# Performance work log

Hardware: AMD Instinct MI355X
Metric: run time of the kernel (lower is better)

The kernel has to match this reference:

```python
import jax, jax.numpy as jnp
import numpy as np
from jax import lax

VOCAB = 32000
D = 256      # d_model
N = 16       # n_neurons
NL = 6       # n_layers
DS = 16      # d_state
DC = 4       # d_conv
DI = 512     # d_inner = expand * d_model
DTR = 16     # dt_rank = ceil(D/16)
NH = 4       # attention heads
HD = D // NH
B, L = 1, 128


def setup_inputs() -> dict:
    key = jax.random.key(0)
    ks = list(jax.random.split(key, 32))
    it = iter(ks)

    def rn(shape, scale):
        return jax.random.normal(next(it), shape, jnp.float32) * scale

    p = {}
    p["x"] = jax.random.randint(next(it), (B, L), 0, VOCAB, dtype=jnp.int32)
    p["embedding"] = rn((VOCAB, D), 0.02)
    p["norm1_w"] = jnp.ones((NL, D)); p["norm1_b"] = jnp.zeros((NL, D))
    p["norm2_w"] = jnp.ones((NL, D)); p["norm2_b"] = jnp.zeros((NL, D))
    # Mamba params (stacked over layers)
    p["in_proj_w"] = rn((NL, 2 * DI, D), D ** -0.5)
    p["conv_w"] = rn((NL, DI, DC), DC ** -0.5)
    p["conv_b"] = jnp.zeros((NL, DI))
    p["x_proj_w"] = rn((NL, DTR + 2 * DS, DI), DI ** -0.5)
    p["dt_proj_w"] = rn((NL, DI, DTR), DTR ** -0.5)
    dt0 = jax.random.uniform(next(it), (NL, DI), jnp.float32, 1e-3, 1e-1)
    p["dt_proj_b"] = jnp.log(jnp.expm1(dt0))  # inverse softplus init
    p["A_log"] = jnp.log(jnp.tile(jnp.arange(1.0, DS + 1.0, dtype=jnp.float32), (NL, DI, 1)))
    p["skip_D"] = jnp.ones((NL, DI))
    p["out_proj_w"] = rn((NL, D, DI), DI ** -0.5)
    # cross-neuron MHA params
    p["attn_in_w"] = rn((NL, 3 * D, D), D ** -0.5)
    p["attn_in_b"] = jnp.zeros((NL, 3 * D))
    p["attn_out_w"] = rn((NL, D, D), D ** -0.5)
    p["attn_out_b"] = jnp.zeros((NL, D))
    p["norm_f_w"] = jnp.ones((D,)); p["norm_f_b"] = jnp.zeros((D,))
    p["head_b"] = jnp.zeros((VOCAB,))
    return p


def _ln(x, w, b):
    m = x.mean(-1, keepdims=True)
    v = ((x - m) ** 2).mean(-1, keepdims=True)
    return (x - m) * lax.rsqrt(v + 1e-5) * w + b


def _mamba(x, ipw, cw, cb, xpw, dpw, dpb, alog, dskip, opw):
    # x: (BN, L, D)
    BN, Ls, _ = x.shape
    xz = x @ ipw.T                       # (BN, L, 2*DI)
    u, z = xz[..., :DI], xz[..., DI:]
    # depthwise causal conv1d, kernel DC, left-pad DC-1
    uc = lax.conv_general_dilated(
        u.swapaxes(1, 2), cw[:, None, :], (1,), [(DC - 1, 0)],
        dimension_numbers=("NCH", "OIH", "NCH"), feature_group_count=DI)
    u = jax.nn.silu(uc + cb[None, :, None]).swapaxes(1, 2)  # (BN, L, DI)
    xdbl = u @ xpw.T                     # (BN, L, DTR+2*DS)
    dt = jax.nn.softplus(xdbl[..., :DTR] @ dpw.T + dpb)     # (BN, L, DI)
    Bm = xdbl[..., DTR:DTR + DS]
    Cm = xdbl[..., DTR + DS:]
    A = -jnp.exp(alog)                   # (DI, DS)

    def step(h, ins):
        dt_t, b_t, c_t, u_t = ins        # (BN,DI) (BN,DS) (BN,DS) (BN,DI)
        h = jnp.exp(dt_t[..., None] * A) * h + (dt_t * u_t)[..., None] * b_t[:, None, :]
        return h, jnp.einsum("bds,bs->bd", h, c_t)

    h0 = jnp.zeros((BN, DI, DS), x.dtype)
    _, ys = lax.scan(step, h0, (dt.swapaxes(0, 1), Bm.swapaxes(0, 1),
                                Cm.swapaxes(0, 1), u.swapaxes(0, 1)))
    y = ys.swapaxes(0, 1) + u * dskip
    return (y * jax.nn.silu(z)) @ opw.T


def _mha(x, iw, ib, ow, ob):
    # x: (B*L, N, D); self-attention across neurons
    Bq, S, _ = x.shape
    qkv = x @ iw.T + ib
    q, k, v = jnp.split(qkv, 3, axis=-1)
    q = q.reshape(Bq, S, NH, HD); k = k.reshape(Bq, S, NH, HD); v = v.reshape(Bq, S, NH, HD)
    att = jax.nn.softmax(jnp.einsum("bqhd,bkhd->bhqk", q, k) / np.float32(np.sqrt(HD)), axis=-1)
    o = jnp.einsum("bhqk,bkhd->bqhd", att, v).reshape(Bq, S, D)
    return o @ ow.T + ob


def reference(x, embedding, norm1_w, norm1_b, norm2_w, norm2_b, in_proj_w, conv_w,
              conv_b, x_proj_w, dt_proj_w, dt_proj_b, A_log, skip_D, out_proj_w,
              attn_in_w, attn_in_b, attn_out_w, attn_out_b, norm_f_w, norm_f_b, head_b):
    Bb, Ll = x.shape
    h = embedding[x]                                             # (B, L, D)
    h = jnp.broadcast_to(h[:, None], (Bb, N, Ll, D)).reshape(Bb * N, Ll, D)
    for i in range(NL):
        h = h + _mamba(_ln(h, norm1_w[i], norm1_b[i]), in_proj_w[i], conv_w[i],
                       conv_b[i], x_proj_w[i], dt_proj_w[i], dt_proj_b[i],
                       A_log[i], skip_D[i], out_proj_w[i])
        xc = _ln(h, norm2_w[i], norm2_b[i]).reshape(Bb, N, Ll, D)
        xc = xc.transpose(0, 2, 1, 3).reshape(Bb * Ll, N, D)
        co = _mha(xc, attn_in_w[i], attn_in_b[i], attn_out_w[i], attn_out_b[i])
        h = h + co.reshape(Bb, Ll, N, D).transpose(0, 2, 1, 3).reshape(Bb * N, Ll, D)
    h = h.reshape(Bb, N, Ll, D).mean(axis=1)                     # avg over neurons
    return _ln(h, norm_f_w, norm_f_b) @ embedding.T + head_b     # tied head
```

## Files before the change

### kernel.cpp

```cpp
#include <hip/hip_runtime.h>

constexpr int SEQ    = 128;
constexpr int NVOCAB = 32000;

constexpr size_t O_HA = 0;
constexpr size_t O_HB = O_HA + (size_t)SEQ*256;
constexpr size_t O_U  = O_HB + (size_t)SEQ*256;
constexpr size_t O_DT = O_U  + (size_t)SEQ*512;
constexpr size_t O_ZS = O_DT + (size_t)SEQ*512;
constexpr size_t O_BC = O_ZS + (size_t)SEQ*512;
constexpr size_t O_YG = O_BC + (size_t)SEQ*32;
constexpr size_t O_AH = O_YG + (size_t)SEQ*512;

__device__ __forceinline__ float wsum(float p) {
    #pragma unroll
    for (int m = 1; m < 64; m <<= 1) p += __shfl_xor(p, m);
    return p;
}
__device__ __forceinline__ float dot4(float4 a, float4 b) {
    return a.x*b.x + a.y*b.y + a.z*b.z + a.w*b.w;
}

template<int MR, int KK>
__device__ __forceinline__ void gemmX(
    const float* __restrict__ Wg, const float* __restrict__ A, int AS,
    float* __restrict__ dest, int DS,
    const float* __restrict__ addsrc, int ASS, const float* __restrict__ bias)
{
    const int lane = threadIdx.x & 63;
    const int wv   = threadIdx.x >> 6;
    const int tq = lane & 3, cs = lane >> 2;
    const int c  = wv*16 + cs;
    const float* Wp = Wg + (size_t)c*KK + tq*8;
    float acc[MR];
    #pragma unroll
    for (int r = 0; r < MR; ++r) acc[r] = 0.0f;

    float4 w0a = *(const float4*)(Wp);
    float4 w0b = *(const float4*)(Wp + 4);
    float4 w1a, w1b;
    #pragma unroll
    for (int kc = 0; kc < KK; kc += 64) {
        if (kc + 32 < KK) {
            w1a = *(const float4*)(Wp + kc + 32);
            w1b = *(const float4*)(Wp + kc + 36);
        }
        #pragma unroll
        for (int r = 0; r < MR; ++r) {
            float4 a0 = *(const float4*)&A[r*AS + kc + tq*8];
            float4 a1 = *(const float4*)&A[r*AS + kc + tq*8 + 4];
            acc[r] += dot4(a0, w0a) + dot4(a1, w0b);
        }
        if (kc + 64 < KK) {
            w0a = *(const float4*)(Wp + kc + 64);
            w0b = *(const float4*)(Wp + kc + 68);
        }
        if (kc + 32 < KK) {
            #pragma unroll
            for (int r = 0; r < MR; ++r) {
                float4 a0 = *(const float4*)&A[r*AS + kc + 32 + tq*8];
                float4 a1 = *(const float4*)&A[r*AS + kc + 36 + tq*8];
                acc[r] += dot4(a0, w1a) + dot4(a1, w1b);
            }
        }
    }
    #pragma unroll
    for (int r = 0; r < MR; ++r) {
        float v = acc[r];
        v += __shfl_xor(v, 1);
        v += __shfl_xor(v, 2);
        acc[r] = v;
    }
    if (tq == 0) {
        #pragma unroll
        for (int r = 0; r < MR; ++r) {
            float v = acc[r];
            if (bias)   v += bias[c];
            if (addsrc) v += addsrc[r*ASS + c];
            dest[r*DS + c] = v;
        }
    }
}

__device__ __forceinline__ void ln_row(const float* __restrict__ src, float* __restrict__ dst,
                                       const float* __restrict__ w, const float* __restrict__ b)
{
    int lane = threadIdx.x & 63;
    float4 x = *(const float4*)&src[lane*4];
    float sm = wsum(x.x + x.y + x.z + x.w);
    float mean = sm * (1.0f/256.0f);
    float d0 = x.x-mean, d1 = x.y-mean, d2 = x.z-mean, d3 = x.w-mean;
    float var = wsum(d0*d0 + d1*d1 + d2*d2 + d3*d3) * (1.0f/256.0f);
    float rstd = rsqrtf(var + 1e-5f);
    float4 ww = *(const float4*)&w[lane*4];
    float4 bb = *(const float4*)&b[lane*4];
    float4 o;
    o.x = d0*rstd*ww.x + bb.x;
    o.y = d1*rstd*ww.y + bb.y;
    o.z = d2*rstd*ww.z + bb.z;
    o.w = d3*rstd*ww.w + bb.w;
    *(float4*)&dst[lane*4] = o;
}

__global__ __launch_bounds__(1024) void rowk_kernel(
    const int* __restrict__ x, const float* __restrict__ emb,
    const float* __restrict__ n1w_l, const float* __restrict__ n1b_l,
    const float* __restrict__ n2w_l, const float* __restrict__ n2b_l,
    const float* __restrict__ ipw_l, const float* __restrict__ cw_l, const float* __restrict__ cb_l,
    const float* __restrict__ xpw_l, const float* __restrict__ dpw_l, const float* __restrict__ dpb_l,
    const float* __restrict__ opw_l, const float* __restrict__ aivw_l, const float* __restrict__ aivb_l,
    const float* __restrict__ aow_l, const float* __restrict__ aob_l,
    const float* __restrict__ nfw, const float* __restrict__ nfb,
    const float* __restrict__ hin, float* __restrict__ hout,
    const float* __restrict__ ygv, float* __restrict__ uv, float* __restrict__ dtv,
    float* __restrict__ zsv, float* __restrict__ bcv, float* __restrict__ AH,
    int li)
{
    __shared__ float SM[6336];
    float* hP  = SM;
    float* h1  = SM + 1056;
    float* sLN = SM + 2112;
    float* sAX = SM + 3168;
    float* zR  = SM + 5248;
    float* suR = SM + 5760;
    float* sxR = SM + 6272;

    const int r = blockIdx.x;
    const int tid = threadIdx.x;
    const int lane = tid & 63, wv = tid >> 6;
    int rr[4];
    #pragma unroll
    for (int j = 0; j < 4; ++j) { int v = r - 3 + j; rr[j] = v < 0 ? 0 : v; }

    {
        int hr = tid >> 8, hc = tid & 255;
        if (li <= 1) hP[hr*264 + hc] = emb[(size_t)x[rr[hr]]*256 + hc];
        else         hP[hr*264 + hc] = hin[rr[hr]*256 + hc];
    }
    __syncthreads();

    float* hC = hP;
    if (li >= 1) {
        {
            int yr = tid >> 9, yc = tid & 511;
            sAX[yr*520 + yc]     = ygv[rr[yr]*512 + yc];
            sAX[(2+yr)*520 + yc] = ygv[rr[2+yr]*512 + yc];
        }
        __syncthreads();
        gemmX<4,512>(opw_l, sAX, 520, h1, 264, hP, 264, nullptr);
        __syncthreads();
        if (wv < 4) ln_row(h1 + wv*264, sLN + wv*264, n2w_l, n2b_l);
        __syncthreads();
        gemmX<4,256>(aivw_l, sLN, 264, sAX, 520, nullptr, 0, aivb_l);
        __syncthreads();
        gemmX<4,256>(aow_l, sAX, 520, h1, 264, h1, 264, aob_l);
        __syncthreads();
        hC = h1;
        if (tid < 256) hout[r*256 + tid] = h1[3*264 + tid];
        if (li == 6) {
            if (tid < 256) {
                float v = h1[3*264 + tid];
                float s = wsum(v);
                float q = wsum(v*v);
                if (lane == 0) { sxR[wv] = s; sxR[8 + wv] = q; }
            }
            __syncthreads();
            if (tid < 256) {
                float v = h1[3*264 + tid];
                float mean = (sxR[0]+sxR[1]+sxR[2]+sxR[3]) * (1.0f/256.0f);
                float var  = (sxR[8]+sxR[9]+sxR[10]+sxR[11]) * (1.0f/256.0f) - mean*mean;
                float rstd = rsqrtf(var + 1e-5f);
                AH[r*256 + tid] = (v - mean)*rstd*nfw[tid] + nfb[tid];
            }
            return;
        }
    }

    if (wv < 4) ln_row(hC + wv*264, sLN + wv*264, n1w_l, n1b_l);
    __syncthreads();
    gemmX<4,256>(ipw_l,                   sLN, 264, sAX,       520, nullptr, 0, nullptr);
    __syncthreads();
    gemmX<4,256>(ipw_l + (size_t)256*256, sLN, 264, sAX + 256, 520, nullptr, 0, nullptr);
    __syncthreads();
    gemmX<1,256>(ipw_l + (size_t)512*256, sLN + 3*264, 264, zR,       512, nullptr, 0, nullptr);
    __syncthreads();
    gemmX<1,256>(ipw_l + (size_t)768*256, sLN + 3*264, 264, zR + 256, 512, nullptr, 0, nullptr);
    __syncthreads();

    if (tid < 512) {
        int d = tid;
        float4 c4 = *(const float4*)&cw_l[d*4];
        float acc = cb_l[d];
        if (r >= 3) acc += sAX[d]        * c4.x;
        if (r >= 2) acc += sAX[520 + d]  * c4.y;
        if (r >= 1) acc += sAX[1040 + d] * c4.z;
        acc += sAX[1560 + d] * c4.w;
        float sg = acc / (1.0f + __expf(-acc));
        suR[d] = sg;
        uv[r*512 + d] = sg;
        float z = zR[d];
        zsv[r*512 + d] = z / (1.0f + __expf(-z));
    }
    __syncthreads();

    {
        float4 a0 = *(const float4*)&suR[lane*4];
        float4 a1 = *(const float4*)&suR[256 + lane*4];
        float p[3];
        #pragma unroll
        for (int j = 0; j < 3; ++j) {
            int c = wv*3 + j;
            float4 q0 = *(const float4*)&xpw_l[(size_t)c*512 + lane*4];
            float4 q1 = *(const float4*)&xpw_l[(size_t)c*512 + 256 + lane*4];
            p[j] = dot4(a0, q0) + dot4(a1, q1);
        }
        #pragma unroll
        for (int m = 1; m < 64; m <<= 1) {
            #pragma unroll
            for (int j = 0; j < 3; ++j) p[j] += __shfl_xor(p[j], m);
        }
        if (lane == 0) {
            #pragma unroll
            for (int j = 0; j < 3; ++j) sxR[wv*3 + j] = p[j];
        }
    }
    __syncthreads();
    if (tid >= 16 && tid < 48) bcv[r*32 + tid - 16] = sxR[tid];

    if (tid < 512) {
        int d = tid;
        float4 sx0 = *(const float4*)&sxR[0];
        float4 sx1 = *(const float4*)&sxR[4];
        float4 sx2 = *(const float4*)&sxR[8];
        float4 sx3 = *(const float4*)&sxR[12];
        const float4* dp = (const float4*)&dpw_l[(size_t)d*16];
        float acc = dpb_l[d] + dot4(dp[0], sx0) + dot4(dp[1], sx1)
                             + dot4(dp[2], sx2) + dot4(dp[3], sx3);
        dtv[r*512 + d] = fmaxf(acc, 0.0f) + log1pf(__expf(-fabsf(acc)));
    }
}

__global__ __launch_bounds__(128) void scan_kernel(
    const float* __restrict__ dt, const float* __restrict__ u, const float* __restrict__ zs,
    const float* __restrict__ bcv,
    const float* __restrict__ alog_l, const float* __restrict__ dsk_l,
    float* __restrict__ yg)
{
    __shared__ float sdt[8*132];
    __shared__ float su2[8*132];
    __shared__ float sz2[8*132];
    __shared__ float sB [16*132];
    __shared__ float sC [16*132];
    const int tid = threadIdx.x;
    const int s  = tid & 15;
    const int dl = tid >> 4;
    const int d0 = blockIdx.x * 8;
    const int d  = d0 + dl;

    {
        const int t = tid;
        float4 q0, q1;
        q0 = *(const float4*)&dt[t*512 + d0];
        q1 = *(const float4*)&dt[t*512 + d0 + 4];
        sdt[0*132+t]=q0.x; sdt[1*132+t]=q0.y; sdt[2*132+t]=q0.z; sdt[3*132+t]=q0.w;
        sdt[4*132+t]=q1.x; sdt[5*132+t]=q1.y; sdt[6*132+t]=q1.z; sdt[7*132+t]=q1.w;
        q0 = *(const float4*)&u[t*512 + d0];
        q1 = *(const float4*)&u[t*512 + d0 + 4];
        su2[0*132+t]=q0.x; su2[1*132+t]=q0.y; su2[2*132+t]=q0.z; su2[3*132+t]=q0.w;
        su2[4*132+t]=q1.x; su2[5*132+t]=q1.y; su2[6*132+t]=q1.z; su2[7*132+t]=q1.w;
        q0 = *(const float4*)&zs[t*512 + d0];
        q1 = *(const float4*)&zs[t*512 + d0 + 4];
        sz2[0*132+t]=q0.x; sz2[1*132+t]=q0.y; sz2[2*132+t]=q0.z; sz2[3*132+t]=q0.w;
        sz2[4*132+t]=q1.x; sz2[5*132+t]=q1.y; sz2[6*132+t]=q1.z; sz2[7*132+t]=q1.w;
        float4 b0 = *(const float4*)&bcv[t*32 + 0];
        float4 b1 = *(const float4*)&bcv[t*32 + 4];
        float4 b2 = *(const float4*)&bcv[t*32 + 8];
        float4 b3 = *(const float4*)&bcv[t*32 + 12];
        sB[ 0*132+t]=b0.x; sB[ 1*132+t]=b0.y; sB[ 2*132+t]=b0.z; sB[ 3*132+t]=b0.w;
        sB[ 4*132+t]=b1.x; sB[ 5*132+t]=b1.y; sB[ 6*132+t]=b1.z; sB[ 7*132+t]=b1.w;
        sB[ 8*132+t]=b2.x; sB[ 9*132+t]=b2.y; sB[10*132+t]=b2.z; sB[11*132+t]=b2.w;
        sB[12*132+t]=b3.x; sB[13*132+t]=b3.y; sB[14*132+t]=b3.z; sB[15*132+t]=b3.w;
        float4 c0 = *(const float4*)&bcv[t*32 + 16];
        float4 c1 = *(const float4*)&bcv[t*32 + 20];
        float4 c2 = *(const float4*)&bcv[t*32 + 24];
        float4 c3 = *(const float4*)&bcv[t*32 + 28];
        sC[ 0*132+t]=c0.x; sC[ 1*132+t]=c0.y; sC[ 2*132+t]=c0.z; sC[ 3*132+t]=c0.w;
        sC[ 4*132+t]=c1.x; sC[ 5*132+t]=c1.y; sC[ 6*132+t]=c1.z; sC[ 7*132+t]=c1.w;
        sC[ 8*132+t]=c2.x; sC[ 9*132+t]=c2.y; sC[10*132+t]=c2.z; sC[11*132+t]=c2.w;
        sC[12*132+t]=c3.x; sC[13*132+t]=c3.y; sC[14*132+t]=c3.z; sC[15*132+t]=c3.w;
    }
    __syncthreads();

    const float a_ds = -__expf(alog_l[d*16 + s]);
    const float dskv = dsk_l[d];
    float hst = 0.0f;
    #pragma unroll 8
    for (int t = 0; t < SEQ; ++t) {
        float dtvv = sdt[dl*132 + t];
        float uvv  = su2[dl*132 + t];
        hst = __expf(dtvv * a_ds) * hst + dtvv * uvv * sB[s*132 + t];
        float p = hst * sC[s*132 + t];
        p += __shfl_xor(p, 1);
        p += __shfl_xor(p, 2);
        p += __shfl_xor(p, 4);
        p += __shfl_xor(p, 8);
        if (s == 0) yg[t*512 + d] = (p + uvv * dskv) * sz2[dl*132 + t];
    }
}

__global__ __launch_bounds__(256) void head_kernel(
    const float* __restrict__ AH, const float* __restrict__ emb,
    const float* __restrict__ hb, float* __restrict__ out)
{
    __shared__ float sA[32*132];
    __shared__ float sW[32*68];
    const int tid = threadIdx.x;
    const int c0  = blockIdx.x * 64;
    const int ar = tid >> 1;
    const int ak = (tid & 1) * 16;
    const int wc = tid & 63;
    const int wk = (tid >> 6) * 8;
    const int rg = tid >> 4;
    const int cg = tid & 15;

    const float* Ap = AH  + (size_t)ar*256 + ak;
    const float* Wp = emb + (size_t)(c0 + wc)*256 + wk;

    float4 ra0 = *(const float4*)(Ap + 0);
    float4 ra1 = *(const float4*)(Ap + 4);
    float4 ra2 = *(const float4*)(Ap + 8);
    float4 ra3 = *(const float4*)(Ap + 12);
    float4 rw0 = *(const float4*)(Wp + 0);
    float4 rw1 = *(const float4*)(Wp + 4);

    float acc[8][4] = {};

    for (int kc = 0; kc < 256; kc += 32) {
        if (kc) __syncthreads();
        sA[(ak+ 0)*132+ar]=ra0.x; sA[(ak+ 1)*132+ar]=ra0.y; sA[(ak+ 2)*132+ar]=ra0.z; sA[(ak+ 3)*132+ar]=ra0.w;
        sA[(ak+ 4)*132+ar]=ra1.x; sA[(ak+ 5)*132+ar]=ra1.y; sA[(ak+ 6)*132+ar]=ra1.z; sA[(ak+ 7)*132+ar]=ra1.w;
        sA[(ak+ 8)*132+ar]=ra2.x; sA[(ak+ 9)*132+ar]=ra2.y; sA[(ak+10)*132+ar]=ra2.z; sA[(ak+11)*132+ar]=ra2.w;
        sA[(ak+12)*132+ar]=ra3.x; sA[(ak+13)*132+ar]=ra3.y; sA[(ak+14)*132+ar]=ra3.z; sA[(ak+15)*132+ar]=ra3.w;
        sW[(wk+0)*68+wc]=rw0.x; sW[(wk+1)*68+wc]=rw0.y; sW[(wk+2)*68+wc]=rw0.z; sW[(wk+3)*68+wc]=rw0.w;
        sW[(wk+4)*68+wc]=rw1.x; sW[(wk+5)*68+wc]=rw1.y; sW[(wk+6)*68+wc]=rw1.z; sW[(wk+7)*68+wc]=rw1.w;
        __syncthreads();
        if (kc + 32 < 256) {
            ra0 = *(const float4*)(Ap + kc + 32);
            ra1 = *(const float4*)(Ap + kc + 36);
            ra2 = *(const float4*)(Ap + kc + 40);
            ra3 = *(const float4*)(Ap + kc + 44);
            rw0 = *(const float4*)(Wp + kc + 32);
            rw1 = *(const float4*)(Wp + kc + 36);
        }
        #pragma unroll
        for (int k = 0; k < 32; ++k) {
            float4 a0 = *(const float4*)&sA[k*132 + rg*8];
            float4 a1 = *(const float4*)&sA[k*132 + rg*8 + 4];
            float4 b  = *(const float4*)&sW[k*68  + cg*4];
            float av[8] = {a0.x,a0.y,a0.z,a0.w, a1.x,a1.y,a1.z,a1.w};
            #pragma unroll
            for (int i = 0; i < 8; ++i) {
                acc[i][0] += av[i]*b.x;
                acc[i][1] += av[i]*b.y;
                acc[i][2] += av[i]*b.z;
                acc[i][3] += av[i]*b.w;
            }
        }
    }

    const int c = c0 + cg*4;
    float4 h4 = *(const float4*)&hb[c];
    #pragma unroll
    for (int i = 0; i < 8; ++i) {
        int r = rg*8 + i;
        float4 o;
        o.x = acc[i][0] + h4.x;
        o.y = acc[i][1] + h4.y;
        o.z = acc[i][2] + h4.z;
        o.w = acc[i][3] + h4.w;
        *(float4*)&out[(size_t)r*NVOCAB + c] = o;
    }
}

extern "C" void kernel_launch(void* const* d_in, const int* in_sizes, int n_in,
                              void* d_out, int out_size, void* d_ws, size_t ws_size,
                              hipStream_t stream)
{
    const int*   xin = (const int*)d_in[0];
    const float* emb = (const float*)d_in[1];
    const float* n1w = (const float*)d_in[2];
    const float* n1b = (const float*)d_in[3];
    const float* n2w = (const float*)d_in[4];
    const float* n2b = (const float*)d_in[5];
    const float* ipw = (const float*)d_in[6];
    const float* cw  = (const float*)d_in[7];
    const float* cb  = (const float*)d_in[8];
    const float* xpw = (const float*)d_in[9];
    const float* dpw = (const float*)d_in[10];
    const float* dpb = (const float*)d_in[11];
    const float* alog= (const float*)d_in[12];
    const float* dsk = (const float*)d_in[13];
    const float* opw = (const float*)d_in[14];
    const float* aiw = (const float*)d_in[15];
    const float* aib = (const float*)d_in[16];
    const float* aow = (const float*)d_in[17];
    const float* aob = (const float*)d_in[18];
    const float* nfw = (const float*)d_in[19];
    const float* nfb = (const float*)d_in[20];
    const float* hb  = (const float*)d_in[21];
    float* ws  = (float*)d_ws;
    float* out = (float*)d_out;

    for (int i = 0; i <= 6; ++i) {
        int ka = i <= 5 ? i : 5;
        int kc = i >= 1 ? i - 1 : 0;
        const float* hin  = (i % 2 == 0) ? ws + O_HA : ws + O_HB;
        float*       hout = (i % 2 == 0) ? ws + O_HB : ws + O_HA;
        rowk_kernel<<<128, 1024, 0, stream>>>(
            xin, emb,
            n1w + ka*256, n1b + ka*256,
            n2w + kc*256, n2b + kc*256,
            ipw + (size_t)ka*1024*256, cw + (size_t)ka*512*4, cb + ka*512,
            xpw + (size_t)ka*48*512, dpw + (size_t)ka*512*16, dpb + ka*512,
            opw + (size_t)kc*256*512,
            aiw + (size_t)kc*768*256 + (size_t)512*256, aib + kc*768 + 512,
            aow + (size_t)kc*256*256, aob + kc*256,
            nfw, nfb,
            hin, hout,
            ws + O_YG, ws + O_U, ws + O_DT, ws + O_ZS, ws + O_BC, ws + O_AH,
            i);
        if (i <= 5)
            scan_kernel<<<64, 128, 0, stream>>>(
                ws + O_DT, ws + O_U, ws + O_ZS, ws + O_BC,
                alog + (size_t)i*512*16, dsk + i*512, ws + O_YG);
    }
    head_kernel<<<NVOCAB/64, 256, 0, stream>>>(ws + O_AH, emb, hb, out);
}
```

Baseline: 538.5 us.

## Restructure per-row GEMV helper to compute four columns per thread with K-split

Replaces the gemmX helper with gemm2, where each thread owns four output columns and a contiguous K slice, so each activation float4 read from shared memory is reused across four weight rows. The in_proj halves are merged into single calls covering 512 columns, cutting two block barriers, and the ygv load is moved ahead of the first barrier to drop one more sync. The cost is more registers per thread for the four accumulator sets and a wider shuffle reduction across the K-split lanes. Weight loads become strided per thread rather than coalesced across lanes, which may change global memory efficiency.

```diff
diff --git a/kernel.cpp b/kernel.cpp
--- a/kernel.cpp
+++ b/kernel.cpp
@@ -21,63 +21,68 @@
     return a.x*b.x + a.y*b.y + a.z*b.z + a.w*b.w;
 }
 
-template<int MR, int KK>
-__device__ __forceinline__ void gemmX(
+template<int MR, int KK, int S>
+__device__ __forceinline__ void gemm2(
     const float* __restrict__ Wg, const float* __restrict__ A, int AS,
     float* __restrict__ dest, int DS,
     const float* __restrict__ addsrc, int ASS, const float* __restrict__ bias)
 {
-    const int lane = threadIdx.x & 63;
-    const int wv   = threadIdx.x >> 6;
-    const int tq = lane & 3, cs = lane >> 2;
-    const int c  = wv*16 + cs;
-    const float* Wp = Wg + (size_t)c*KK + tq*8;
-    float acc[MR];
-    #pragma unroll
-    for (int r = 0; r < MR; ++r) acc[r] = 0.0f;
-
-    float4 w0a = *(const float4*)(Wp);
-    float4 w0b = *(const float4*)(Wp + 4);
-    float4 w1a, w1b;
-    #pragma unroll
-    for (int kc = 0; kc < KK; kc += 64) {
-        if (kc + 32 < KK) {
-            w1a = *(const float4*)(Wp + kc + 32);
-            w1b = *(const float4*)(Wp + kc + 36);
-        }
+    constexpr int KS  = KK / S;
+    constexpr int NST = KS / 4;
+    const int tid = threadIdx.x;
+    const int tq  = tid & (S - 1);
+    const int c0  = (tid / S) * 4;
+    const float* Wp = Wg + (size_t)c0 * KK + tq * KS;
+
+    float acc0[MR], acc1[MR], acc2[MR], acc3[MR];
+    #pragma unroll
+    for (int r = 0; r < MR; ++r) { acc0[r]=0.f; acc1[r]=0.f; acc2[r]=0.f; acc3[r]=0.f; }
+
+    float4 w0 = *(const float4*)(Wp);
+    float4 w1 = *(const float4*)(Wp + KK);
+    float4 w2 = *(const float4*)(Wp + 2*KK);
+    float4 w3 = *(const float4*)(Wp + 3*KK);
+    #pragma unroll
+    for (int st = 0; st < NST; ++st) {
+        float4 n0, n1, n2, n3;
+        if (st + 1 < NST) {
+            n0 = *(const float4*)(Wp + (st+1)*4);
+            n1 = *(const float4*)(Wp + KK + (st+1)*4);
+            n2 = *(const float4*)(Wp + 2*KK + (st+1)*4);
+            n3 = *(const float4*)(Wp + 3*KK + (st+1)*4);
+        }
+        const int k = tq*KS + st*4;
         #pragma unroll
         for (int r = 0; r < MR; ++r) {
-            float4 a0 = *(const float4*)&A[r*AS + kc + tq*8];
-            float4 a1 = *(const float4*)&A[r*AS + kc + tq*8 + 4];
-            acc[r] += dot4(a0, w0a) + dot4(a1, w0b);
-        }
-        if (kc + 64 < KK) {
-            w0a = *(const float4*)(Wp + kc + 64);
-            w0b = *(const float4*)(Wp + kc + 68);
-        }
-        if (kc + 32 < KK) {
-            #pragma unroll
-            for (int r = 0; r < MR; ++r) {
-                float4 a0 = *(const float4*)&A[r*AS + kc + 32 + tq*8];
-                float4 a1 = *(const float4*)&A[r*AS + kc + 36 + tq*8];
-                acc[r] += dot4(a0, w1a) + dot4(a1, w1b);
+            float4 a = *(const float4*)&A[r*AS + k];
+            acc0[r] += dot4(a, w0);
+            acc1[r] += dot4(a, w1);
+            acc2[r] += dot4(a, w2);
+            acc3[r] += dot4(a, w3);
+        }
+        if (st + 1 < NST) { w0 = n0; w1 = n1; w2 = n2; w3 = n3; }
+    }
+    #pragma unroll
+    for (int m = 1; m < S; m <<= 1) {
+        #pragma unroll
+        for (int r = 0; r < MR; ++r) {
+            acc0[r] += __shfl_xor(acc0[r], m);
+            acc1[r] += __shfl_xor(acc1[r], m);
+            acc2[r] += __shfl_xor(acc2[r], m);
+            acc3[r] += __shfl_xor(acc3[r], m);
+        }
+    }
+    if (tq == 0) {
+        #pragma unroll
+        for (int r = 0; r < MR; ++r) {
+            float ox = acc0[r], oy = acc1[r], oz = acc2[r], ow = acc3[r];
+            if (bias) { ox += bias[c0]; oy += bias[c0+1]; oz += bias[c0+2]; ow += bias[c0+3]; }
+            if (addsrc) {
+                float4 s = *(const float4*)&addsrc[r*ASS + c0];
+                ox += s.x; oy += s.y; oz += s.z; ow += s.w;
             }
-        }
-    }
-    #pragma unroll
-    for (int r = 0; r < MR; ++r) {
-        float v = acc[r];
-        v += __shfl_xor(v, 1);
-        v += __shfl_xor(v, 2);
-        acc[r] = v;
-    }
-    if (tq == 0) {
-        #pragma unroll
-        for (int r = 0; r < MR; ++r) {
-            float v = acc[r];
-            if (bias)   v += bias[c];
-            if (addsrc) v += addsrc[r*ASS + c];
-            dest[r*DS + c] = v;
+            float4 o; o.x = ox; o.y = oy; o.z = oz; o.w = ow;
+            *(float4*)&dest[r*DS + c0] = o;
         }
     }
 }
@@ -137,23 +142,22 @@
         if (li <= 1) hP[hr*264 + hc] = emb[(size_t)x[rr[hr]]*256 + hc];
         else         hP[hr*264 + hc] = hin[rr[hr]*256 + hc];
     }
+    if (li >= 1) {
+        int yr = tid >> 9, yc = tid & 511;
+        sAX[yr*520 + yc]     = ygv[rr[yr]*512 + yc];
+        sAX[(2+yr)*520 + yc] = ygv[rr[2+yr]*512 + yc];
+    }
     __syncthreads();
 
     float* hC = hP;
     if (li >= 1) {
-        {
-            int yr = tid >> 9, yc = tid & 511;
-            sAX[yr*520 + yc]     = ygv[rr[yr]*512 + yc];
-            sAX[(2+yr)*520 + yc] = ygv[rr[2+yr]*512 + yc];
-        }
-        __syncthreads();
-        gemmX<4,512>(opw_l, sAX, 520, h1, 264, hP, 264, nullptr);
+        gemm2<4,512,16>(opw_l, sAX, 520, h1, 264, hP, 264, nullptr);
         __syncthreads();
         if (wv < 4) ln_row(h1 + wv*264, sLN + wv*264, n2w_l, n2b_l);
         __syncthreads();
-        gemmX<4,256>(aivw_l, sLN, 264, sAX, 520, nullptr, 0, aivb_l);
+        gemm2<4,256,16>(aivw_l, sLN, 264, sAX, 520, nullptr, 0, aivb_l);
         __syncthreads();
-        gemmX<4,256>(aow_l, sAX, 520, h1, 264, h1, 264, aob_l);
+        gemm2<4,256,16>(aow_l, sAX, 520, h1, 264, h1, 264, aob_l);
         __syncthreads();
         hC = h1;
         if (tid < 256) hout[r*256 + tid] = h1[3*264 + tid];
@@ -178,13 +182,8 @@
 
     if (wv < 4) ln_row(hC + wv*264, sLN + wv*264, n1w_l, n1b_l);
     __syncthreads();
-    gemmX<4,256>(ipw_l,                   sLN, 264, sAX,       520, nullptr, 0, nullptr);
-    __syncthreads();
-    gemmX<4,256>(ipw_l + (size_t)256*256, sLN, 264, sAX + 256, 520, nullptr, 0, nullptr);
-    __syncthreads();
-    gemmX<1,256>(ipw_l + (size_t)512*256, sLN + 3*264, 264, zR,       512, nullptr, 0, nullptr);
-    __syncthreads();
-    gemmX<1,256>(ipw_l + (size_t)768*256, sLN + 3*264, 264, zR + 256, 512, nullptr, 0, nullptr);
+    gemm2<4,256,8>(ipw_l,                   sLN,         264, sAX, 520, nullptr, 0, nullptr);
+    gemm2<1,256,8>(ipw_l + (size_t)512*256, sLN + 3*264, 264, zR,  512, nullptr, 0, nullptr);
     __syncthreads();
 
     if (tid < 512) {
```

After: 1.033 ms. +91.7%, slower.
